# Optimization experiments

Hardware: AMD Instinct MI355X
Metric: run time of the kernel (lower is better)

## Reference

```python
import jax, jax.numpy as jnp
import numpy as np

N_EMBED = 1024
N_HEADS = 16
CTX = 2048
B, T = 4, 2048
HD = N_EMBED // N_HEADS


def setup_inputs() -> dict:
    key = jax.random.key(0)
    ks = jax.random.split(key, 5)
    scale = 1.0 / np.sqrt(N_EMBED)
    return {
        "x": jax.random.normal(ks[0], (B, T, N_EMBED), dtype=jnp.float32),
        "wq": jax.random.normal(ks[1], (N_EMBED, N_EMBED), dtype=jnp.float32) * scale,
        "wk": jax.random.normal(ks[2], (N_EMBED, N_EMBED), dtype=jnp.float32) * scale,
        "wv": jax.random.normal(ks[3], (N_EMBED, N_EMBED), dtype=jnp.float32) * scale,
        "wo": jax.random.normal(ks[4], (N_EMBED, N_EMBED), dtype=jnp.float32) * scale,
    }


def reference(x, wq, wk, wv, wo):
    b, t, c = x.shape
    # nn.Linear applies x @ W.T ; split heads -> [B, H, T, hd]
    def proj(w):
        return jnp.einsum("btc,dc->btd", x, w).reshape(b, t, N_HEADS, HD).transpose(0, 2, 1, 3)
    q, k, v = proj(wq), proj(wk), proj(wv)
    scores = jnp.einsum("bhqd,bhkd->bhqk", q, k) * (HD ** -0.5)
    causal = jnp.tril(jnp.ones((t, t), dtype=bool))
    scores = jnp.where(causal[None, None, :, :], scores, -jnp.inf)
    a = jax.nn.softmax(scores, axis=-1)
    o = jnp.einsum("bhqk,bhkd->bhqd", a, v)  # [B,H,T,hd]
    o = o.transpose(0, 2, 1, 3).reshape(b, t, c)
    return jnp.einsum("btc,dc->btd", o, wo)
```

## Files before the change

kernel.cpp:

```cpp
#include <hip/hip_runtime.h>
#include <stdint.h>


typedef __attribute__((ext_vector_type(8))) short bf16x8;
typedef __attribute__((ext_vector_type(4))) float f32x4;
typedef __attribute__((ext_vector_type(16))) float f32x16;
typedef unsigned short us;
typedef unsigned int u32;

#define LOG2E 1.4426950408889634f

#define GL2LDS16(g, l)                                                          \
  __builtin_amdgcn_global_load_lds(                                             \
      (const __attribute__((address_space(1))) unsigned int*)(g),               \
      (__attribute__((address_space(3))) unsigned int*)(l), 16, 0, 0)

__device__ inline us f2bf(float f) {
  union { float f; unsigned int u; } v; v.f = f;
  unsigned int u = v.u;
  u += 0x7FFFu + ((u >> 16) & 1u);
  return (us)(u >> 16);
}

__global__ void cast_all(const float* __restrict__ x,
                         const float* __restrict__ w0, const float* __restrict__ w1,
                         const float* __restrict__ w2, const float* __restrict__ w3,
                         us* __restrict__ xb, us* __restrict__ wbuf) {
  int i = (blockIdx.x * blockDim.x + threadIdx.x) * 8;
  const float* src;
  us* dst;
  float sc = 1.0f;
  if (i < (8 << 20)) {
    src = x + i; dst = xb + i;
  } else {
    int j = i - (8 << 20);
    int seg = j >> 20;
    int off = j & ((1 << 20) - 1);
    const float* w = (seg == 0) ? w0 : (seg == 1) ? w1 : (seg == 2) ? w2 : w3;
    if (seg == 0) sc = 0.125f * LOG2E;
    src = w + off; dst = wbuf + j;
  }
  float4 a = *reinterpret_cast<const float4*>(src);
  float4 b = *reinterpret_cast<const float4*>(src + 4);
  union { us u[8]; uint4 v; } o;
  o.u[0] = f2bf(a.x * sc); o.u[1] = f2bf(a.y * sc);
  o.u[2] = f2bf(a.z * sc); o.u[3] = f2bf(a.w * sc);
  o.u[4] = f2bf(b.x * sc); o.u[5] = f2bf(b.y * sc);
  o.u[6] = f2bf(b.z * sc); o.u[7] = f2bf(b.w * sc);
  *reinterpret_cast<uint4*>(dst) = o.v;
}

__global__ __launch_bounds__(256, 2) void gemm_qkv(
    const us* __restrict__ A, const us* __restrict__ Bw,
    us* __restrict__ QKV, us* __restrict__ Vt) {
  const int K = 1024, N = 3072;
  __shared__ __align__(16) us Al[128 * 64];
  __shared__ __align__(16) us Bl[128 * 64];
  const int tid = threadIdx.x;
  const int lane = tid & 63;
  const int w = tid >> 6;
  const int quad = lane >> 4;
  const int l16 = lane & 15;
  const int m0 = blockIdx.y * 128;
  const int n0 = blockIdx.x * 128;
  const int wm = w >> 1, wn = w & 1;
  const int srow_base = w * 8 + (lane >> 3);
  const int sunit = lane & 7;
  f32x4 acc[4][4] = {};

  for (int k0 = 0; k0 < K; k0 += 64) {
    __syncthreads();
#pragma unroll
    for (int it = 0; it < 4; ++it) {
      int row = it * 32 + srow_base;
      int gu = sunit ^ (row & 7);
      int base = __builtin_amdgcn_readfirstlane((it * 256 + w * 64) * 8);
      GL2LDS16(A + (size_t)(m0 + row) * K + k0 + gu * 8, &Al[base]);
      GL2LDS16(Bw + (size_t)(n0 + row) * K + k0 + gu * 8, &Bl[base]);
    }
    __syncthreads();
#pragma unroll
    for (int kk = 0; kk < 2; ++kk) {
      bf16x8 af[4], bfr[4];
#pragma unroll
      for (int mi = 0; mi < 4; ++mi) {
        int row = wm * 64 + mi * 16 + l16;
        af[mi] = *reinterpret_cast<const bf16x8*>(
            &Al[row * 64 + (((kk * 4 + quad) ^ (row & 7)) * 8)]);
      }
#pragma unroll
      for (int ni = 0; ni < 4; ++ni) {
        int row = wn * 64 + ni * 16 + l16;
        bfr[ni] = *reinterpret_cast<const bf16x8*>(
            &Bl[row * 64 + (((kk * 4 + quad) ^ (row & 7)) * 8)]);
      }
#pragma unroll
      for (int mi = 0; mi < 4; ++mi)
#pragma unroll
        for (int ni = 0; ni < 4; ++ni)
          acc[mi][ni] = __builtin_amdgcn_mfma_f32_16x16x32_bf16(af[mi], bfr[ni], acc[mi][ni], 0, 0, 0);
    }
  }

  if (n0 < 2048) {
#pragma unroll
    for (int mi = 0; mi < 4; ++mi)
#pragma unroll
      for (int ni = 0; ni < 4; ++ni)
#pragma unroll
        for (int r = 0; r < 4; ++r) {
          int row = m0 + wm * 64 + mi * 16 + quad * 4 + r;
          int col = n0 + wn * 64 + ni * 16 + l16;
          QKV[(size_t)row * N + col] = f2bf(acc[mi][ni][r]);
        }
  } else {
    const int bI = m0 >> 11;
    const int tbase = m0 & 2047;
#pragma unroll
    for (int mi = 0; mi < 4; ++mi)
#pragma unroll
      for (int ni = 0; ni < 4; ++ni)
#pragma unroll
        for (int r = 0; r < 4; ++r) {
          int krow = tbase + wm * 64 + mi * 16 + quad * 4 + r;
          int col = n0 + wn * 64 + ni * 16 + l16;
          int hh = (col - 2048) >> 6;
          int d = col & 63;
          Vt[((size_t)((bI * 16 + hh) * 64 + d)) * 2048 + krow] = f2bf(acc[mi][ni][r]);
        }
  }
}

__global__ __launch_bounds__(256, 2) void gemm_out(
    const us* __restrict__ A, const us* __restrict__ Bw,
    float* __restrict__ Cv, int M, int N, int K) {
  __shared__ __align__(16) us Al[128 * 64];
  __shared__ __align__(16) us Bl[128 * 64];
  const int tid = threadIdx.x;
  const int lane = tid & 63;
  const int w = tid >> 6;
  const int quad = lane >> 4;
  const int l16 = lane & 15;
  const int m0 = blockIdx.y * 128;
  const int n0 = blockIdx.x * 128;
  const int wm = w >> 1, wn = w & 1;
  const int srow_base = w * 8 + (lane >> 3);
  const int sunit = lane & 7;
  f32x4 acc[4][4] = {};

  for (int k0 = 0; k0 < K; k0 += 64) {
    __syncthreads();
#pragma unroll
    for (int it = 0; it < 4; ++it) {
      int row = it * 32 + srow_base;
      int gu = sunit ^ (row & 7);
      int base = __builtin_amdgcn_readfirstlane((it * 256 + w * 64) * 8);
      GL2LDS16(A + (size_t)(m0 + row) * K + k0 + gu * 8, &Al[base]);
      GL2LDS16(Bw + (size_t)(n0 + row) * K + k0 + gu * 8, &Bl[base]);
    }
    __syncthreads();
#pragma unroll
    for (int kk = 0; kk < 2; ++kk) {
      bf16x8 af[4], bfr[4];
#pragma unroll
      for (int mi = 0; mi < 4; ++mi) {
        int row = wm * 64 + mi * 16 + l16;
        af[mi] = *reinterpret_cast<const bf16x8*>(
            &Al[row * 64 + (((kk * 4 + quad) ^ (row & 7)) * 8)]);
      }
#pragma unroll
      for (int ni = 0; ni < 4; ++ni) {
        int row = wn * 64 + ni * 16 + l16;
        bfr[ni] = *reinterpret_cast<const bf16x8*>(
            &Bl[row * 64 + (((kk * 4 + quad) ^ (row & 7)) * 8)]);
      }
#pragma unroll
      for (int mi = 0; mi < 4; ++mi)
#pragma unroll
        for (int ni = 0; ni < 4; ++ni)
          acc[mi][ni] = __builtin_amdgcn_mfma_f32_16x16x32_bf16(af[mi], bfr[ni], acc[mi][ni], 0, 0, 0);
    }
  }

#pragma unroll
  for (int mi = 0; mi < 4; ++mi)
#pragma unroll
    for (int ni = 0; ni < 4; ++ni)
#pragma unroll
      for (int r = 0; r < 4; ++r) {
        int row = m0 + wm * 64 + mi * 16 + quad * 4 + r;
        int col = n0 + wn * 64 + ni * 16 + l16;
        Cv[(size_t)row * N + col] = acc[mi][ni][r];
      }
}

__global__ __launch_bounds__(256, 3) void attn(
    const us* __restrict__ QKV, const us* __restrict__ Vt,
    us* __restrict__ O) {
  __shared__ __align__(16) us Kb[2][64 * 64];
  __shared__ __align__(16) us Vb[2][64 * 64];
  __shared__ float Ls[4][32];
  const int bid = blockIdx.x;
  const int j16 = bid >> 6;
  const int grp = j16 >> 2, pos = j16 & 3;
  const int qt = (grp == 0) ? 15 - pos : (grp == 1) ? pos
               : (grp == 2) ? 11 - pos : 4 + pos;
  const int bh = bid & 63;
  const int b = bh >> 4, h = bh & 15;
  const int q0 = qt * 128;
  const int tid = threadIdx.x, lane = tid & 63, w = tid >> 6;
  const int l31 = lane & 31, hi = lane >> 5;
  const size_t rowbase = (size_t)b * 2048;
  const int qcol = h * 64;
  const int kcol = 1024 + h * 64;
  const int qw = q0 + w * 32;
  const int nT = 2 * qt + 2;

  const int mr = (l31 & 7) ^ ((l31 >> 3) & 3);

  bf16x8 qf[4];
#pragma unroll
  for (int ds = 0; ds < 4; ++ds)
    qf[ds] = *reinterpret_cast<const bf16x8*>(
        &QKV[(rowbase + qw + l31) * 3072 + qcol + ds * 16 + hi * 8]);

  f32x16 oacc[2] = {};
  float psum = 0.f;

  const int rr8 = w * 8 + (lane >> 3);
  const int ms = (rr8 & 7) ^ ((rr8 >> 3) & 3);
  const int uu = lane & 7;
  const int gu = uu ^ ms;

  auto stage = [&](int kt, int buf) {
#pragma unroll
    for (int c = 0; c < 2; ++c) {
      int row = c * 32 + rr8;
      int base = __builtin_amdgcn_readfirstlane((c * 32 + w * 8) * 64);
      GL2LDS16(QKV + (rowbase + kt * 64 + row) * 3072 + kcol + gu * 8,
               &Kb[buf][base]);
      GL2LDS16(Vt + ((size_t)(bh * 64 + row)) * 2048 + kt * 64 + gu * 8,
               &Vb[buf][base]);
    }
  };

  stage(0, 0);

  for (int kt = 0; kt < nT; ++kt) {
    asm volatile("s_waitcnt vmcnt(0)" ::: "memory");
    asm volatile("s_barrier" ::: "memory");
    if (kt + 1 < nT) stage(kt + 1, (kt + 1) & 1);
    const us* Kl = &Kb[kt & 1][0];
    const us* Vl = &Vb[kt & 1][0];

    const int kdiff = qw + 31 - kt * 64;
    if (kdiff < 0) continue;
    const int tmax = (kdiff >= 32) ? 2 : 1;
    const bool do_mask = (kt * 64 + 63) > qw;

#pragma unroll
    for (int t = 0; t < 2; ++t) {
      if (t < tmax) {
        f32x16 s = {};
#pragma unroll
        for (int ds = 0; ds < 4; ++ds) {
          int row = t * 32 + l31;
          bf16x8 kf = *reinterpret_cast<const bf16x8*>(
              &Kl[row * 64 + (((ds * 2 + hi) ^ mr) * 8)]);
          s = __builtin_amdgcn_mfma_f32_32x32x16_bf16(kf, qf[ds], s, 0, 0, 0);
        }

        float p[16];
        if (do_mask) {
#pragma unroll
          for (int r = 0; r < 16; ++r) {
            float e = __builtin_amdgcn_exp2f(s[r]);
            int kg = kt * 64 + t * 32 + (r & 3) + ((r >> 2) << 3) + hi * 4;
            p[r] = (kg <= qw + l31) ? e : 0.f;
            psum += p[r];
          }
        } else {
#pragma unroll
          for (int r = 0; r < 16; ++r) {
            p[r] = __builtin_amdgcn_exp2f(s[r]);
            psum += p[r];
          }
        }

        u32 pk[4][2];
#pragma unroll
        for (int bb = 0; bb < 4; ++bb)
#pragma unroll
          for (int w2 = 0; w2 < 2; ++w2)
            asm("v_cvt_pk_bf16_f32 %0, %1, %2"
                : "=v"(pk[bb][w2])
                : "v"(p[4 * bb + 2 * w2]), "v"(p[4 * bb + 2 * w2 + 1]));

#pragma unroll
        for (int s2 = 0; s2 < 2; ++s2) {
          u32 pa[4];
#pragma unroll
          for (int w2 = 0; w2 < 2; ++w2) {
            u32 a = pk[2 * s2][w2];
            u32 c = pk[2 * s2 + 1][w2];
            asm volatile("v_permlane32_swap_b32 %0, %1" : "+v"(a), "+v"(c));
            pa[w2] = a;
            pa[2 + w2] = c;
          }
          union { u32 u[4]; bf16x8 v; } pu;
          pu.u[0] = pa[0]; pu.u[1] = pa[1]; pu.u[2] = pa[2]; pu.u[3] = pa[3];
          bf16x8 paf = pu.v;
          int ks = t * 2 + s2;
#pragma unroll
          for (int dt = 0; dt < 2; ++dt) {
            int row = dt * 32 + l31;
            bf16x8 vf = *reinterpret_cast<const bf16x8*>(
                &Vl[row * 64 + (((ks * 2 + hi) ^ mr) * 8)]);
            oacc[dt] = __builtin_amdgcn_mfma_f32_32x32x16_bf16(paf, vf, oacc[dt], 0, 0, 0);
          }
        }
      }
    }
  }

  {
    float a = psum, c = psum;
    asm volatile("v_permlane32_swap_b32 %0, %1" : "+v"(a), "+v"(c));
    float invl = 1.0f / (a + c);
    if (!hi) Ls[w][l31] = invl;
    asm volatile("s_waitcnt lgkmcnt(0)" ::: "memory");
  }
  float inv[16];
#pragma unroll
  for (int r = 0; r < 16; ++r)
    inv[r] = Ls[w][(r & 3) + ((r >> 2) << 3) + hi * 4];
#pragma unroll
  for (int dt = 0; dt < 2; ++dt)
#pragma unroll
    for (int r = 0; r < 16; ++r) {
      int qg = qw + (r & 3) + ((r >> 2) << 3) + hi * 4;
      O[(rowbase + qg) * 1024 + qcol + dt * 32 + l31] = f2bf(oacc[dt][r] * inv[r]);
    }
}

extern "C" void kernel_launch(void* const* d_in, const int* in_sizes, int n_in,
                              void* d_out, int out_size, void* d_ws, size_t ws_size,
                              hipStream_t stream) {
  const float* x = (const float*)d_in[0];
  const float* wq = (const float*)d_in[1];
  const float* wk = (const float*)d_in[2];
  const float* wv = (const float*)d_in[3];
  const float* wo = (const float*)d_in[4];

  const int BT = 8192, E = 1024;
  const size_t NX = (size_t)BT * E;
  const size_t NW = (size_t)E * E;

  us* xb = (us*)d_ws;
  us* wbuf = xb + NX;
  us* QKV = wbuf + 4 * NW;
  us* VtB = QKV + (size_t)BT * 3 * E;
  us* Ob = xb;

  cast_all<<<(int)((NX + 4 * NW) / 8 / 256), 256, 0, stream>>>(x, wq, wk, wv, wo, xb, wbuf);

  gemm_qkv<<<dim3(24, 64), 256, 0, stream>>>(xb, wbuf, QKV, VtB);
  attn<<<1024, 256, 0, stream>>>(QKV, VtB, Ob);
  gemm_out<<<dim3(8, 64), 256, 0, stream>>>(Ob, wbuf + 3 * NW, (float*)d_out, BT, E, E);
}
```

Baseline: 225.3 us.

## Rewrite QKV GEMM with 256x256 tiles and 4-stage async LDS pipeline

The QKV projection GEMM moves from 128x128 tiles with 4 waves to 256x256 tiles with 8 waves, using a 4-stage ring buffer of direct global-to-LDS loads with explicit vmcnt waits so loads overlap MFMA work. Block IDs are swizzled for L2 locality and MFMA sections are bracketed by setprio. The larger tile cuts global traffic per FLOP and barrier overhead. In exchange it uses 128KB of LDS and more accumulator registers, which lowers occupancy, and the 384-block grid may leave CUs unevenly loaded.

```diff
diff --git a/kernel.cpp b/kernel.cpp
--- a/kernel.cpp
+++ b/kernel.cpp
@@ -50,66 +50,94 @@
   *reinterpret_cast<uint4*>(dst) = o.v;
 }
 
-__global__ __launch_bounds__(256, 2) void gemm_qkv(
+__global__ __launch_bounds__(512, 2) void gemm_qkv256(
     const us* __restrict__ A, const us* __restrict__ Bw,
     us* __restrict__ QKV, us* __restrict__ Vt) {
   const int K = 1024, N = 3072;
-  __shared__ __align__(16) us Al[128 * 64];
-  __shared__ __align__(16) us Bl[128 * 64];
+  __shared__ __align__(16) us As[4][8192];
+  __shared__ __align__(16) us Bs[4][8192];
   const int tid = threadIdx.x;
   const int lane = tid & 63;
   const int w = tid >> 6;
-  const int quad = lane >> 4;
-  const int l16 = lane & 15;
-  const int m0 = blockIdx.y * 128;
-  const int n0 = blockIdx.x * 128;
-  const int wm = w >> 1, wn = w & 1;
-  const int srow_base = w * 8 + (lane >> 3);
-  const int sunit = lane & 7;
-  f32x4 acc[4][4] = {};
-
-  for (int k0 = 0; k0 < K; k0 += 64) {
-    __syncthreads();
-#pragma unroll
-    for (int it = 0; it < 4; ++it) {
-      int row = it * 32 + srow_base;
-      int gu = sunit ^ (row & 7);
-      int base = __builtin_amdgcn_readfirstlane((it * 256 + w * 64) * 8);
-      GL2LDS16(A + (size_t)(m0 + row) * K + k0 + gu * 8, &Al[base]);
-      GL2LDS16(Bw + (size_t)(n0 + row) * K + k0 + gu * 8, &Bl[base]);
-    }
-    __syncthreads();
-#pragma unroll
-    for (int kk = 0; kk < 2; ++kk) {
-      bf16x8 af[4], bfr[4];
-#pragma unroll
-      for (int mi = 0; mi < 4; ++mi) {
-        int row = wm * 64 + mi * 16 + l16;
-        af[mi] = *reinterpret_cast<const bf16x8*>(
-            &Al[row * 64 + (((kk * 4 + quad) ^ (row & 7)) * 8)]);
-      }
-#pragma unroll
-      for (int ni = 0; ni < 4; ++ni) {
-        int row = wn * 64 + ni * 16 + l16;
-        bfr[ni] = *reinterpret_cast<const bf16x8*>(
-            &Bl[row * 64 + (((kk * 4 + quad) ^ (row & 7)) * 8)]);
-      }
-#pragma unroll
-      for (int mi = 0; mi < 4; ++mi)
-#pragma unroll
-        for (int ni = 0; ni < 4; ++ni)
-          acc[mi][ni] = __builtin_amdgcn_mfma_f32_16x16x32_bf16(af[mi], bfr[ni], acc[mi][ni], 0, 0, 0);
-    }
+  const int wm = w >> 2, wn = w & 3;
+  const int quad = lane >> 4, l16 = lane & 15;
+
+  const int bid = blockIdx.x;
+  const int swz = (bid & 7) * 48 + (bid >> 3);
+  const int mt = swz / 12, nt = swz % 12;
+  const int m0 = mt * 256, n0 = nt * 256;
+
+  const int j3 = (tid >> 3) & 7;
+  const int upre = (tid & 7) ^ j3;
+  const int Rb = ((tid >> 3) << 1) | (upre >> 2);
+  const int kof = (upre & 3) * 8;
+  const size_t arow0 = (size_t)(m0 + Rb) * K + kof;
+  const size_t arow1 = (size_t)(m0 + Rb + 128) * K + kof;
+  const size_t brow0 = (size_t)(n0 + Rb) * K + kof;
+  const size_t brow1 = (size_t)(n0 + Rb + 128) * K + kof;
+  const int wofs = __builtin_amdgcn_readfirstlane(w * 512);
+
+  const int lrow = (l16 >> 1) * 64 +
+                   ((((l16 & 1) * 4 + quad) ^ ((l16 >> 1) & 7)) * 8);
+
+  f32x4 acc[8][4] = {};
+
+  auto stage = [&](int ss, int ks) {
+    const int sb = ss * 8192;
+    GL2LDS16(A + arow0 + ks * 32, &As[0][sb + wofs]);
+    GL2LDS16(A + arow1 + ks * 32, &As[0][sb + 4096 + wofs]);
+    GL2LDS16(Bw + brow0 + ks * 32, &Bs[0][sb + wofs]);
+    GL2LDS16(Bw + brow1 + ks * 32, &Bs[0][sb + 4096 + wofs]);
+  };
+
+  stage(0, 0);
+  stage(1, 1);
+  stage(2, 2);
+
+#pragma unroll 1
+  for (int s = 0; s < 32; ++s) {
+    if (s < 29) {
+      stage((s + 3) & 3, s + 3);
+      asm volatile("s_waitcnt vmcnt(12)" ::: "memory");
+    } else if (s == 29) {
+      asm volatile("s_waitcnt vmcnt(8)" ::: "memory");
+    } else if (s == 30) {
+      asm volatile("s_waitcnt vmcnt(4)" ::: "memory");
+    } else {
+      asm volatile("s_waitcnt vmcnt(0)" ::: "memory");
+    }
+    asm volatile("s_barrier" ::: "memory");
+
+    const int sb = (s & 3) * 8192;
+    bf16x8 af[8], bf[4];
+#pragma unroll
+    for (int mi = 0; mi < 8; ++mi)
+      af[mi] = *reinterpret_cast<const bf16x8*>(
+          &As[0][sb + wm * 4096 + mi * 512 + lrow]);
+#pragma unroll
+    for (int ni = 0; ni < 4; ++ni)
+      bf[ni] = *reinterpret_cast<const bf16x8*>(
+          &Bs[0][sb + wn * 2048 + ni * 512 + lrow]);
+
+    __builtin_amdgcn_s_setprio(1);
+#pragma unroll
+    for (int mi = 0; mi < 8; ++mi)
+#pragma unroll
+      for (int ni = 0; ni < 4; ++ni)
+        acc[mi][ni] = __builtin_amdgcn_mfma_f32_16x16x32_bf16(af[mi], bf[ni], acc[mi][ni], 0, 0, 0);
+    __builtin_amdgcn_s_setprio(0);
+
+    asm volatile("s_barrier" ::: "memory");
   }
 
   if (n0 < 2048) {
 #pragma unroll
-    for (int mi = 0; mi < 4; ++mi)
+    for (int mi = 0; mi < 8; ++mi)
 #pragma unroll
       for (int ni = 0; ni < 4; ++ni)
 #pragma unroll
         for (int r = 0; r < 4; ++r) {
-          int row = m0 + wm * 64 + mi * 16 + quad * 4 + r;
+          int row = m0 + wm * 128 + mi * 16 + quad * 4 + r;
           int col = n0 + wn * 64 + ni * 16 + l16;
           QKV[(size_t)row * N + col] = f2bf(acc[mi][ni][r]);
         }
@@ -117,12 +145,12 @@
     const int bI = m0 >> 11;
     const int tbase = m0 & 2047;
 #pragma unroll
-    for (int mi = 0; mi < 4; ++mi)
+    for (int mi = 0; mi < 8; ++mi)
 #pragma unroll
       for (int ni = 0; ni < 4; ++ni)
 #pragma unroll
         for (int r = 0; r < 4; ++r) {
-          int krow = tbase + wm * 64 + mi * 16 + quad * 4 + r;
+          int krow = tbase + wm * 128 + mi * 16 + quad * 4 + r;
           int col = n0 + wn * 64 + ni * 16 + l16;
           int hh = (col - 2048) >> 6;
           int d = col & 63;
@@ -364,7 +392,7 @@
 
   cast_all<<<(int)((NX + 4 * NW) / 8 / 256), 256, 0, stream>>>(x, wq, wk, wv, wo, xb, wbuf);
 
-  gemm_qkv<<<dim3(24, 64), 256, 0, stream>>>(xb, wbuf, QKV, VtB);
+  gemm_qkv256<<<384, 512, 0, stream>>>(xb, wbuf, QKV, VtB);
   attn<<<1024, 256, 0, stream>>>(QKV, VtB, Ob);
   gemm_out<<<dim3(8, 64), 256, 0, stream>>>(Ob, wbuf + 3 * NW, (float*)d_out, BT, E, E);
 }
```

Measured after the change: 244.2 us. +8.4%, slower.
